# Kernel optimization log

Hardware: AMD Instinct MI355X
Metric: run time of the kernel (lower is better)

The kernel has to match this reference:

```python
import jax, jax.numpy as jnp
import numpy as np

N, F, H, L, O, E = 20000, 128, 128, 4, 64, 640000
NEG_SLOPE = 0.2  # PyG GATConv default


def setup_inputs() -> dict:
    key = jax.random.key(0)
    ks = jax.random.split(key, 8)
    x = jax.random.normal(ks[0], (N, F), dtype=jnp.float32)
    edge_index = jax.random.randint(ks[1], (2, E), 0, N, dtype=jnp.int64)
    sc = 1.0 / np.sqrt(F)
    Ws = jax.random.normal(ks[2], (L, F, H), dtype=jnp.float32) * sc
    att_src = jax.random.normal(ks[3], (L, H), dtype=jnp.float32) * sc
    att_dst = jax.random.normal(ks[4], (L, H), dtype=jnp.float32) * sc
    biases = jnp.zeros((L, H), dtype=jnp.float32)
    W_out = jax.random.normal(ks[5], (H, O), dtype=jnp.float32) * (1.0 / np.sqrt(H))
    b_out = jnp.zeros((O,), dtype=jnp.float32)
    return {"x": x, "edge_index": edge_index, "Ws": Ws, "att_src": att_src,
            "att_dst": att_dst, "biases": biases, "W_out": W_out, "b_out": b_out}


def _gat_conv(h, src, dst, W, a_s, a_d, b):
    # h: [N, F_in]; single-head GATConv (PyG semantics)
    z = h @ W                                   # [N, H]
    alpha_s = z @ a_s                           # [N]
    alpha_d = z @ a_d                           # [N]
    logits = jax.nn.leaky_relu(alpha_s[src] + alpha_d[dst], negative_slope=NEG_SLOPE)  # [E']
    # segment-softmax over edges grouped by destination node
    m = jax.ops.segment_max(logits, dst, num_segments=N)
    p = jnp.exp(logits - m[dst])
    s = jax.ops.segment_sum(p, dst, num_segments=N)
    alpha = p / (s[dst] + 1e-16)                # [E']
    out = jax.ops.segment_sum(alpha[:, None] * z[src], dst, num_segments=N)  # [N, H]
    return out + b


def reference(x, edge_index, Ws, att_src, att_dst, biases, W_out, b_out):
    # add self-loops once (PyG GATConv default add_self_loops=True)
    loop = jnp.arange(N, dtype=edge_index.dtype)
    src = jnp.concatenate([edge_index[0], loop])
    dst = jnp.concatenate([edge_index[1], loop])
    h = x
    for l in range(L):
        h = _gat_conv(h, src, dst, Ws[l], att_src[l], att_dst[l], biases[l])
        h = jax.nn.relu(h)  # Dropout is identity at eval
    return h @ W_out + b_out  # [N, O]
```

## Files before the change

kernel.cpp:

```cpp
#include <hip/hip_runtime.h>

#define NN 20000
#define FF 128
#define HH 128
#define LL 4
#define OO 64
#define EE 640000
#define NEG 0.2f
#define NB ((NN + 255) / 256)


__global__ void k_init_counters(int* __restrict__ counters) {
    int i = blockIdx.x * 256 + threadIdx.x;
    if (i < NN) counters[i] = 1;
}

__global__ void k_hist(const int* __restrict__ dst, int* __restrict__ counters) {
    int e = blockIdx.x * 256 + threadIdx.x;
    if (e < EE) atomicAdd(&counters[dst[e]], 1);
}

__global__ void k_partial(const int* __restrict__ counters, int* __restrict__ partials) {
    __shared__ int ws[4];
    int t = threadIdx.x;
    int i = blockIdx.x * 256 + t;
    int c = (i < NN) ? counters[i] : 0;
    #pragma unroll
    for (int off = 32; off; off >>= 1) c += __shfl_xor(c, off);
    if ((t & 63) == 0) ws[t >> 6] = c;
    __syncthreads();
    if (t == 0) partials[blockIdx.x] = ws[0] + ws[1] + ws[2] + ws[3];
}

__global__ void k_scan_small(const int* __restrict__ partials, int* __restrict__ offsets) {
    __shared__ int sp[128];
    int t = threadIdx.x;
    int v = (t < NB) ? partials[t] : 0;
    sp[t] = v;
    __syncthreads();
    for (int off = 1; off < 128; off <<= 1) {
        int u = (t >= off) ? sp[t - off] : 0;
        __syncthreads();
        sp[t] += u;
        __syncthreads();
    }
    if (t < NB) offsets[t] = sp[t] - v;
}

__global__ void k_apply(const int* __restrict__ counters, const int* __restrict__ offsets,
                        int* __restrict__ row_off, int* __restrict__ cursor,
                        int* __restrict__ src_sorted) {
    __shared__ int sc[256];
    int t = threadIdx.x;
    int i = blockIdx.x * 256 + t;
    int c = (i < NN) ? counters[i] : 0;
    sc[t] = c;
    __syncthreads();
    for (int off = 1; off < 256; off <<= 1) {
        int u = (t >= off) ? sc[t - off] : 0;
        __syncthreads();
        sc[t] += u;
        __syncthreads();
    }
    int incl = sc[t];
    int base = offsets[blockIdx.x];
    if (i < NN) {
        int excl = base + incl - c;
        row_off[i] = excl;
        cursor[i] = excl + 1;
        src_sorted[excl] = i;
        if (i == NN - 1) row_off[NN] = base + incl;
    }
}

__global__ void k_scatter(const int* __restrict__ src, const int* __restrict__ dst,
                          int* __restrict__ cursor, int* __restrict__ src_sorted) {
    int e = blockIdx.x * 256 + threadIdx.x;
    if (e < EE) {
        int p = atomicAdd(&cursor[dst[e]], 1);
        src_sorted[p] = src[e];
    }
}


template <int NCOL, bool BIAS, bool ALPHAS>
__global__ void k_gemm(const float* __restrict__ A, const float* __restrict__ W,
                       const float* __restrict__ bias, float* __restrict__ C,
                       const float* __restrict__ a_s, const float* __restrict__ a_d,
                       float* __restrict__ as_out, float* __restrict__ ad_out) {
    constexpr int KB = 32;
    constexpr int CG = NCOL / 4;
    constexpr int TR = 256 / CG;
    constexpr int RPT = 64 / TR;
    __shared__ float sA[64][KB];
    __shared__ float sW[KB][NCOL];

    int t = threadIdx.x;
    int row0 = blockIdx.x * 64;
    int cg = t % CG, tr = t / CG;
    int c0 = cg * 4;

    float acc[RPT][4] = {};

    for (int k0 = 0; k0 < 128; k0 += KB) {
        for (int i = t; i < 64 * KB / 4; i += 256) {
            int r = (i * 4) / KB, kk = (i * 4) % KB;
            float4 v;
            if (row0 + r < NN)
                v = *(const float4*)&A[(size_t)(row0 + r) * 128 + k0 + kk];
            else
                v = make_float4(0.f, 0.f, 0.f, 0.f);
            *(float4*)&sA[r][kk] = v;
        }
        for (int i = t; i < KB * NCOL / 4; i += 256) {
            int r = (i * 4) / NCOL, c = (i * 4) % NCOL;
            *(float4*)&sW[r][c] = *(const float4*)&W[(size_t)(k0 + r) * NCOL + c];
        }
        __syncthreads();

        #pragma unroll
        for (int k = 0; k < KB; k++) {
            float wv[4];
            *(float4*)wv = *(const float4*)&sW[k][c0];
            #pragma unroll
            for (int r = 0; r < RPT; r++) {
                float av = sA[tr * RPT + r][k];
                acc[r][0] += av * wv[0];
                acc[r][1] += av * wv[1];
                acc[r][2] += av * wv[2];
                acc[r][3] += av * wv[3];
            }
        }
        __syncthreads();
    }

    #pragma unroll
    for (int r = 0; r < RPT; r++) {
        int row = row0 + tr * RPT + r;
        if (row < NN) {
            float4 v = make_float4(acc[r][0], acc[r][1], acc[r][2], acc[r][3]);
            if (BIAS) {
                v.x += bias[c0 + 0];
                v.y += bias[c0 + 1];
                v.z += bias[c0 + 2];
                v.w += bias[c0 + 3];
            }
            *(float4*)&C[(size_t)row * NCOL + c0] = v;
        }
    }

    if constexpr (ALPHAS) {
        float4 asv = *(const float4*)&a_s[c0];
        float4 adv = *(const float4*)&a_d[c0];
        #pragma unroll
        for (int r = 0; r < RPT; r++) {
            float ps = acc[r][0] * asv.x + acc[r][1] * asv.y +
                       acc[r][2] * asv.z + acc[r][3] * asv.w;
            float pd = acc[r][0] * adv.x + acc[r][1] * adv.y +
                       acc[r][2] * adv.z + acc[r][3] * adv.w;
            #pragma unroll
            for (int off = 16; off; off >>= 1) {
                ps += __shfl_xor(ps, off);
                pd += __shfl_xor(pd, off);
            }
            int row = row0 + tr * RPT + r;
            if (cg == 0 && row < NN) {
                as_out[row] = ps;
                ad_out[row] = pd;
            }
        }
    }
}


__global__ void k_aggregate(const float* __restrict__ z, const float* __restrict__ as,
                            const float* __restrict__ ad, const int* __restrict__ row_off,
                            const int* __restrict__ srcs, const float* __restrict__ bias,
                            float* __restrict__ out) {
    int node = blockIdx.x * 4 + (threadIdx.x >> 6);
    int lane = threadIdx.x & 63;
    if (node >= NN) return;
    int beg = row_off[node], end = row_off[node + 1];
    float adn = ad[node];

    float mx = -1e30f;
    for (int e = beg + lane; e < end; e += 64) {
        float l = as[srcs[e]] + adn;
        l = (l >= 0.f) ? l : NEG * l;
        mx = fmaxf(mx, l);
    }
    #pragma unroll
    for (int off = 32; off; off >>= 1) mx = fmaxf(mx, __shfl_xor(mx, off));

    int g = lane >> 5, cl = lane & 31;
    const float4* zb = (const float4*)z;
    float4 acc = make_float4(0.f, 0.f, 0.f, 0.f);
    float s = 0.f;
    int e = beg + g;
    for (; e + 6 < end; e += 8) {
        int s0 = srcs[e], s1 = srcs[e + 2], s2 = srcs[e + 4], s3 = srcs[e + 6];
        float l0 = as[s0] + adn; l0 = (l0 >= 0.f) ? l0 : NEG * l0;
        float l1 = as[s1] + adn; l1 = (l1 >= 0.f) ? l1 : NEG * l1;
        float l2 = as[s2] + adn; l2 = (l2 >= 0.f) ? l2 : NEG * l2;
        float l3 = as[s3] + adn; l3 = (l3 >= 0.f) ? l3 : NEG * l3;
        float4 z0 = zb[(size_t)s0 * 32 + cl];
        float4 z1 = zb[(size_t)s1 * 32 + cl];
        float4 z2 = zb[(size_t)s2 * 32 + cl];
        float4 z3 = zb[(size_t)s3 * 32 + cl];
        float p0 = __expf(l0 - mx), p1 = __expf(l1 - mx);
        float p2 = __expf(l2 - mx), p3 = __expf(l3 - mx);
        s += (p0 + p1) + (p2 + p3);
        acc.x += p0 * z0.x + p1 * z1.x + p2 * z2.x + p3 * z3.x;
        acc.y += p0 * z0.y + p1 * z1.y + p2 * z2.y + p3 * z3.y;
        acc.z += p0 * z0.z + p1 * z1.z + p2 * z2.z + p3 * z3.z;
        acc.w += p0 * z0.w + p1 * z1.w + p2 * z2.w + p3 * z3.w;
    }
    for (; e < end; e += 2) {
        int s0 = srcs[e];
        float l0 = as[s0] + adn; l0 = (l0 >= 0.f) ? l0 : NEG * l0;
        float4 z0 = zb[(size_t)s0 * 32 + cl];
        float p0 = __expf(l0 - mx);
        s += p0;
        acc.x += p0 * z0.x;
        acc.y += p0 * z0.y;
        acc.z += p0 * z0.z;
        acc.w += p0 * z0.w;
    }

    acc.x += __shfl_xor(acc.x, 32);
    acc.y += __shfl_xor(acc.y, 32);
    acc.z += __shfl_xor(acc.z, 32);
    acc.w += __shfl_xor(acc.w, 32);
    s     += __shfl_xor(s, 32);

    if (g == 0) {
        float inv = 1.f / (s + 1e-16f);
        float4 b = ((const float4*)bias)[cl];
        float4 o;
        o.x = fmaxf(acc.x * inv + b.x, 0.f);
        o.y = fmaxf(acc.y * inv + b.y, 0.f);
        o.z = fmaxf(acc.z * inv + b.z, 0.f);
        o.w = fmaxf(acc.w * inv + b.w, 0.f);
        ((float4*)out)[(size_t)node * 32 + cl] = o;
    }
}


extern "C" void kernel_launch(void* const* d_in, const int* in_sizes, int n_in,
                              void* d_out, int out_size, void* d_ws, size_t ws_size,
                              hipStream_t stream) {
    const float* x      = (const float*)d_in[0];
    const int*   ei     = (const int*)d_in[1];
    const float* Ws     = (const float*)d_in[2];
    const float* attS   = (const float*)d_in[3];
    const float* attD   = (const float*)d_in[4];
    const float* biases = (const float*)d_in[5];
    const float* W_out  = (const float*)d_in[6];
    const float* b_out  = (const float*)d_in[7];
    float* out = (float*)d_out;

    const int* srcp = ei;
    const int* dstp = ei + EE;

    char* w = (char*)d_ws;
    auto take = [&](size_t bytes) {
        char* p = w;
        w += (bytes + 15) & ~(size_t)15;
        return p;
    };
    float* zbuf       = (float*)take((size_t)NN * HH * 4);
    float* hbuf       = (float*)take((size_t)NN * HH * 4);
    float* as_v       = (float*)take((size_t)NN * 4);
    float* ad_v       = (float*)take((size_t)NN * 4);
    int*   counters   = (int*)take((size_t)NN * 4);
    int*   row_off    = (int*)take((size_t)(NN + 1) * 4);
    int*   cursor     = (int*)take((size_t)NN * 4);
    int*   src_sorted = (int*)take((size_t)(EE + NN) * 4);
    int*   partials   = (int*)take((size_t)NB * 4);
    int*   offsets    = (int*)take((size_t)NB * 4);

    k_init_counters<<<(NN + 255) / 256, 256, 0, stream>>>(counters);
    k_hist<<<(EE + 255) / 256, 256, 0, stream>>>(dstp, counters);
    k_partial<<<NB, 256, 0, stream>>>(counters, partials);
    k_scan_small<<<1, 128, 0, stream>>>(partials, offsets);
    k_apply<<<NB, 256, 0, stream>>>(counters, offsets, row_off, cursor, src_sorted);
    k_scatter<<<(EE + 255) / 256, 256, 0, stream>>>(srcp, dstp, cursor, src_sorted);

    const int gemm_blocks = (NN + 63) / 64;
    const int node_blocks = (NN + 3) / 4;

    for (int l = 0; l < LL; l++) {
        const float* hin = (l == 0) ? x : hbuf;
        k_gemm<HH, false, true><<<gemm_blocks, 256, 0, stream>>>(
            hin, Ws + (size_t)l * FF * HH, nullptr, zbuf,
            attS + l * HH, attD + l * HH, as_v, ad_v);
        k_aggregate<<<node_blocks, 256, 0, stream>>>(zbuf, as_v, ad_v, row_off, src_sorted,
                                                     biases + l * HH, hbuf);
    }

    k_gemm<OO, true, false><<<gemm_blocks, 256, 0, stream>>>(
        hbuf, W_out, b_out, out, nullptr, nullptr, nullptr, nullptr);
}
```

Measured before the change: 340.3 us.

## Drop softmax max pass, unroll aggregation by eight, stream GEMM weights from registers

The aggregation kernel no longer does a separate pass over each node's edges to find the segment max. It shifts the exponentials by the node's self-loop logit instead, which softmax's shift invariance allows. The edge loop is unrolled to eight gathers per iteration, with clamped indices and masked weights replacing the scalar tail loop. The GEMM now loads the full 64x128 A tile into shared memory once and reads W float4s straight from global with register prefetching, which removes the per-K-chunk shared staging and barriers. The self-loop shift risks exp overflow when neighbor logits far exceed the self logit, and reading W from global relies on cache hits.

Result: slower. 412.2 us (+21.1%).

```diff
diff --git a/kernel.cpp b/kernel.cpp
--- a/kernel.cpp
+++ b/kernel.cpp
@@ -88,50 +88,47 @@
                        const float* __restrict__ bias, float* __restrict__ C,
                        const float* __restrict__ a_s, const float* __restrict__ a_d,
                        float* __restrict__ as_out, float* __restrict__ ad_out) {
-    constexpr int KB = 32;
     constexpr int CG = NCOL / 4;
     constexpr int TR = 256 / CG;
     constexpr int RPT = 64 / TR;
-    __shared__ float sA[64][KB];
-    __shared__ float sW[KB][NCOL];
+    __shared__ float sA[64][128];
 
     int t = threadIdx.x;
     int row0 = blockIdx.x * 64;
     int cg = t % CG, tr = t / CG;
     int c0 = cg * 4;
 
+    for (int i = t; i < 2048; i += 256) {
+        int r = i >> 5, c4 = (i & 31) << 2;
+        float4 v = make_float4(0.f, 0.f, 0.f, 0.f);
+        if (row0 + r < NN) v = *(const float4*)&A[(size_t)(row0 + r) * 128 + c4];
+        *(float4*)&sA[r][c4] = v;
+    }
+    __syncthreads();
+
     float acc[RPT][4] = {};
 
-    for (int k0 = 0; k0 < 128; k0 += KB) {
-        for (int i = t; i < 64 * KB / 4; i += 256) {
-            int r = (i * 4) / KB, kk = (i * 4) % KB;
-            float4 v;
-            if (row0 + r < NN)
-                v = *(const float4*)&A[(size_t)(row0 + r) * 128 + k0 + kk];
-            else
-                v = make_float4(0.f, 0.f, 0.f, 0.f);
-            *(float4*)&sA[r][kk] = v;
+    auto ldw = [&](int k) { return *(const float4*)&W[(size_t)k * NCOL + c0]; };
+    auto kstep = [&](float4 wv, int k) {
+        #pragma unroll
+        for (int r = 0; r < RPT; r++) {
+            float av = sA[tr * RPT + r][k];
+            acc[r][0] += av * wv.x;
+            acc[r][1] += av * wv.y;
+            acc[r][2] += av * wv.z;
+            acc[r][3] += av * wv.w;
         }
-        for (int i = t; i < KB * NCOL / 4; i += 256) {
-            int r = (i * 4) / NCOL, c = (i * 4) % NCOL;
-            *(float4*)&sW[r][c] = *(const float4*)&W[(size_t)(k0 + r) * NCOL + c];
-        }
-        __syncthreads();
-
-        #pragma unroll
-        for (int k = 0; k < KB; k++) {
-            float wv[4];
-            *(float4*)wv = *(const float4*)&sW[k][c0];
-            #pragma unroll
-            for (int r = 0; r < RPT; r++) {
-                float av = sA[tr * RPT + r][k];
-                acc[r][0] += av * wv[0];
-                acc[r][1] += av * wv[1];
-                acc[r][2] += av * wv[2];
-                acc[r][3] += av * wv[3];
-            }
-        }
-        __syncthreads();
+    };
+
+    float4 w0 = ldw(0), w1 = ldw(1), w2 = ldw(2), w3 = ldw(3);
+    for (int k0 = 0; k0 < 128; k0 += 4) {
+        int kn = (k0 + 4 < 128) ? (k0 + 4) : k0;
+        float4 n0 = ldw(kn), n1 = ldw(kn + 1), n2 = ldw(kn + 2), n3 = ldw(kn + 3);
+        kstep(w0, k0);
+        kstep(w1, k0 + 1);
+        kstep(w2, k0 + 2);
+        kstep(w3, k0 + 3);
+        w0 = n0; w1 = n1; w2 = n2; w3 = n3;
     }
 
     #pragma unroll
@@ -182,49 +179,53 @@
     if (node >= NN) return;
     int beg = row_off[node], end = row_off[node + 1];
     float adn = ad[node];
-
-    float mx = -1e30f;
-    for (int e = beg + lane; e < end; e += 64) {
-        float l = as[srcs[e]] + adn;
-        l = (l >= 0.f) ? l : NEG * l;
-        mx = fmaxf(mx, l);
-    }
-    #pragma unroll
-    for (int off = 32; off; off >>= 1) mx = fmaxf(mx, __shfl_xor(mx, off));
+    float lself = as[node] + adn;
+    float mx = (lself >= 0.f) ? lself : NEG * lself;
 
     int g = lane >> 5, cl = lane & 31;
     const float4* zb = (const float4*)z;
     float4 acc = make_float4(0.f, 0.f, 0.f, 0.f);
     float s = 0.f;
-    int e = beg + g;
-    for (; e + 6 < end; e += 8) {
-        int s0 = srcs[e], s1 = srcs[e + 2], s2 = srcs[e + 4], s3 = srcs[e + 6];
-        float l0 = as[s0] + adn; l0 = (l0 >= 0.f) ? l0 : NEG * l0;
-        float l1 = as[s1] + adn; l1 = (l1 >= 0.f) ? l1 : NEG * l1;
-        float l2 = as[s2] + adn; l2 = (l2 >= 0.f) ? l2 : NEG * l2;
-        float l3 = as[s3] + adn; l3 = (l3 >= 0.f) ? l3 : NEG * l3;
+
+    for (int e = beg + g; e < end; e += 16) {
+        int e1 = e + 2, e2 = e + 4, e3 = e + 6, e4 = e + 8, e5 = e + 10, e6 = e + 12, e7 = e + 14;
+        int lim = end - 1;
+        int i0 = e;
+        int i1 = min(e1, lim), i2 = min(e2, lim), i3 = min(e3, lim);
+        int i4 = min(e4, lim), i5 = min(e5, lim), i6 = min(e6, lim), i7 = min(e7, lim);
+        int s0 = srcs[i0], s1 = srcs[i1], s2 = srcs[i2], s3 = srcs[i3];
+        int s4 = srcs[i4], s5 = srcs[i5], s6 = srcs[i6], s7 = srcs[i7];
+        float l0 = as[s0] + adn, l1 = as[s1] + adn, l2 = as[s2] + adn, l3 = as[s3] + adn;
+        float l4 = as[s4] + adn, l5 = as[s5] + adn, l6 = as[s6] + adn, l7 = as[s7] + adn;
+        l0 = (l0 >= 0.f) ? l0 : NEG * l0;  l1 = (l1 >= 0.f) ? l1 : NEG * l1;
+        l2 = (l2 >= 0.f) ? l2 : NEG * l2;  l3 = (l3 >= 0.f) ? l3 : NEG * l3;
+        l4 = (l4 >= 0.f) ? l4 : NEG * l4;  l5 = (l5 >= 0.f) ? l5 : NEG * l5;
+        l6 = (l6 >= 0.f) ? l6 : NEG * l6;  l7 = (l7 >= 0.f) ? l7 : NEG * l7;
         float4 z0 = zb[(size_t)s0 * 32 + cl];
         float4 z1 = zb[(size_t)s1 * 32 + cl];
         float4 z2 = zb[(size_t)s2 * 32 + cl];
         float4 z3 = zb[(size_t)s3 * 32 + cl];
-        float p0 = __expf(l0 - mx), p1 = __expf(l1 - mx);
-        float p2 = __expf(l2 - mx), p3 = __expf(l3 - mx);
-        s += (p0 + p1) + (p2 + p3);
-        acc.x += p0 * z0.x + p1 * z1.x + p2 * z2.x + p3 * z3.x;
-        acc.y += p0 * z0.y + p1 * z1.y + p2 * z2.y + p3 * z3.y;
-        acc.z += p0 * z0.z + p1 * z1.z + p2 * z2.z + p3 * z3.z;
-        acc.w += p0 * z0.w + p1 * z1.w + p2 * z2.w + p3 * z3.w;
-    }
-    for (; e < end; e += 2) {
-        int s0 = srcs[e];
-        float l0 = as[s0] + adn; l0 = (l0 >= 0.f) ? l0 : NEG * l0;
-        float4 z0 = zb[(size_t)s0 * 32 + cl];
+        float4 z4 = zb[(size_t)s4 * 32 + cl];
+        float4 z5 = zb[(size_t)s5 * 32 + cl];
+        float4 z6 = zb[(size_t)s6 * 32 + cl];
+        float4 z7 = zb[(size_t)s7 * 32 + cl];
         float p0 = __expf(l0 - mx);
-        s += p0;
-        acc.x += p0 * z0.x;
-        acc.y += p0 * z0.y;
-        acc.z += p0 * z0.z;
-        acc.w += p0 * z0.w;
+        float p1 = (e1 < end) ? __expf(l1 - mx) : 0.f;
+        float p2 = (e2 < end) ? __expf(l2 - mx) : 0.f;
+        float p3 = (e3 < end) ? __expf(l3 - mx) : 0.f;
+        float p4 = (e4 < end) ? __expf(l4 - mx) : 0.f;
+        float p5 = (e5 < end) ? __expf(l5 - mx) : 0.f;
+        float p6 = (e6 < end) ? __expf(l6 - mx) : 0.f;
+        float p7 = (e7 < end) ? __expf(l7 - mx) : 0.f;
+        s += ((p0 + p1) + (p2 + p3)) + ((p4 + p5) + (p6 + p7));
+        acc.x += (p0 * z0.x + p1 * z1.x + p2 * z2.x + p3 * z3.x)
+               + (p4 * z4.x + p5 * z5.x + p6 * z6.x + p7 * z7.x);
+        acc.y += (p0 * z0.y + p1 * z1.y + p2 * z2.y + p3 * z3.y)
+               + (p4 * z4.y + p5 * z5.y + p6 * z6.y + p7 * z7.y);
+        acc.z += (p0 * z0.z + p1 * z1.z + p2 * z2.z + p3 * z3.z)
+               + (p4 * z4.z + p5 * z5.z + p6 * z6.z + p7 * z7.z);
+        acc.w += (p0 * z0.w + p1 * z1.w + p2 * z2.w + p3 * z3.w)
+               + (p4 * z4.w + p5 * z5.w + p6 * z6.w + p7 * z7.w);
     }
 
     acc.x += __shfl_xor(acc.x, 32);
```
